# Kernel optimization log

Measured on AMD Instinct MI355X. Metric: run time of the kernel, lower is better.

The kernel has to match this reference:

```python
import jax, jax.numpy as jnp
import numpy as np

B, L, D = 2, 2048, 1024
H, DK, DV = 16, 64, 64
EPS = 1e-6


def setup_inputs() -> dict:
    key = jax.random.key(0)
    ks = jax.random.split(key, 7)
    s = 0.02
    return {
        "x": jax.random.normal(ks[0], (B, L, D), dtype=jnp.float32),
        "Wq": jax.random.normal(ks[1], (D, H * DK), dtype=jnp.float32) * s,
        "Wk": jax.random.normal(ks[2], (D, H * DK), dtype=jnp.float32) * s,
        "Wv": jax.random.normal(ks[3], (D, H * DV), dtype=jnp.float32) * s,
        "Wo": jax.random.normal(ks[4], (H * DV, D), dtype=jnp.float32) * s,
        "ln_gamma": jnp.ones((D,), dtype=jnp.float32),
        "ln_beta": jnp.zeros((D,), dtype=jnp.float32),
    }


def reference(x, Wq, Wk, Wv, Wo, ln_gamma, ln_beta):
    temp = jnp.asarray(DK, x.dtype) ** 0.5
    # projections -> [B, H, L, Dh]
    q = (x @ Wq).reshape(B, L, H, DK).transpose(0, 2, 1, 3)
    k = (x @ Wk).reshape(B, L, H, DK).transpose(0, 2, 1, 3)
    v = (x @ Wv).reshape(B, L, H, DV).transpose(0, 2, 1, 3)
    # naive attention: explicit [B,H,L,L] scores (dropout rate 0 -> identity)
    scores = jnp.einsum("bhqd,bhkd->bhqk", q / temp, k)
    attn = jax.nn.softmax(scores, axis=-1)
    o = jnp.einsum("bhqk,bhkd->bhqd", attn, v)
    o = o.transpose(0, 2, 1, 3).reshape(B, L, H * DV)
    out = o @ Wo + x  # residual
    # LayerNorm(eps=1e-6)
    mu = jnp.mean(out, axis=-1, keepdims=True)
    var = jnp.var(out, axis=-1, keepdims=True)
    return (out - mu) * jax.lax.rsqrt(var + EPS) * ln_gamma + ln_beta
```

## Files before the change

### kernel.cpp

```cpp
#include <hip/hip_runtime.h>


typedef __bf16 bf16;
typedef __bf16 bf16x2 __attribute__((ext_vector_type(2)));
typedef __bf16 bf16x4 __attribute__((ext_vector_type(4)));
typedef __bf16 bf16x8 __attribute__((ext_vector_type(8)));
typedef float floatx4 __attribute__((ext_vector_type(4)));
typedef int intx4 __attribute__((ext_vector_type(4)));

#define MFMA16(a, b, c) __builtin_amdgcn_mfma_f32_16x16x32_bf16((a), (b), (c), 0, 0, 0)

__device__ __forceinline__ void gll16(const bf16* g, bf16* l) {
  __builtin_amdgcn_global_load_lds((const __attribute__((address_space(1))) void*)g,
                                   (__attribute__((address_space(3))) void*)l, 16, 0, 0);
}

__global__ __launch_bounds__(256) void k_prep(const float* __restrict__ x,
                                              const float* __restrict__ Wq, const float* __restrict__ Wk,
                                              const float* __restrict__ Wv, const float* __restrict__ Wo,
                                              bf16* __restrict__ xb, bf16* __restrict__ WT) {
  __shared__ float tile[32][33];
  const int z = blockIdx.z;
  const int tx = threadIdx.x, ty = threadIdx.y;
  if (z < 4) {
    const float* W = (z == 0) ? Wq : (z == 1) ? Wk : (z == 2) ? Wv : Wo;
    const int n0 = blockIdx.x * 32, k0 = blockIdx.y * 32;
#pragma unroll
    for (int j = 0; j < 32; j += 8)
      tile[ty + j][tx] = W[(size_t)(k0 + ty + j) * 1024 + n0 + tx];
    __syncthreads();
#pragma unroll
    for (int j = 0; j < 32; j += 8)
      WT[(size_t)(z * 1024 + n0 + ty + j) * 1024 + k0 + tx] = (bf16)tile[tx][ty + j];
  } else {
    const int blin = blockIdx.y * 32 + blockIdx.x;
    const int tid = ty * 32 + tx;
    const size_t i = (((size_t)(z - 4) * 1024 + blin) * 256 + tid) * 4;
    const float4 v = *reinterpret_cast<const float4*>(x + i);
    bf16x4 o = {(bf16)v.x, (bf16)v.y, (bf16)v.z, (bf16)v.w};
    *reinterpret_cast<bf16x4*>(xb + i) = o;
  }
}

template <int MODE>
__global__ __launch_bounds__(256) void k_gemm(const bf16* __restrict__ A, const bf16* __restrict__ Bt,
                                              const float* __restrict__ X, float* __restrict__ Y,
                                              bf16* __restrict__ QB, bf16* __restrict__ KB,
                                              bf16* __restrict__ VTB) {
  __shared__ __align__(16) bf16 As[2 * 128 * 64];
  __shared__ __align__(16) bf16 Bs[2 * 128 * 64];
  const int t = threadIdx.x;
  const int lane = t & 63, wv = t >> 6;
  const int qd = lane >> 4, col = lane & 15;
  const int c7 = col & 7;
  const int wm = wv >> 1, wn = wv & 1;
  const int m0 = blockIdx.x * 128, n0 = blockIdx.y * 128;
  const int srow = wv * 8 + (lane >> 3);
  const int scol = ((lane & 7) ^ (lane >> 3)) * 8;
  const bf16* Ag = A + (size_t)(m0 + srow) * 1024 + scol;
  const bf16* Bg = Bt + (size_t)(n0 + srow) * 1024 + scol;

  floatx4 acc[4][4] = {};

#define GSTAGE(bu, ti)                                                                              \
  do {                                                                                              \
    _Pragma("unroll") for (int rd = 0; rd < 4; rd++) {                                              \
      gll16(Ag + (size_t)rd * 32 * 1024 + (ti) * 64, As + (bu) * 8192 + (rd * 32 + wv * 8) * 64);   \
      gll16(Bg + (size_t)rd * 32 * 1024 + (ti) * 64, Bs + (bu) * 8192 + (rd * 32 + wv * 8) * 64);   \
    }                                                                                               \
  } while (0)

#define GCOMP(bu)                                                                                   \
  do {                                                                                              \
    const bf16* as_ = As + (bu) * 8192;                                                             \
    const bf16* bs_ = Bs + (bu) * 8192;                                                             \
    _Pragma("unroll") for (int ks = 0; ks < 2; ks++) {                                              \
      bf16x8 af[4], bfr[4];                                                                         \
      _Pragma("unroll") for (int i = 0; i < 4; i++)                                                 \
        af[i] = *reinterpret_cast<const bf16x8*>(as_ + (wm * 64 + i * 16 + col) * 64 +              \
                                                 ((ks * 4 + qd) ^ c7) * 8);                         \
      _Pragma("unroll") for (int i = 0; i < 4; i++)                                                 \
        bfr[i] = *reinterpret_cast<const bf16x8*>(bs_ + (wn * 64 + i * 16 + col) * 64 +             \
                                                  ((ks * 4 + qd) ^ c7) * 8);                        \
      _Pragma("unroll") for (int i = 0; i < 4; i++)                                                 \
        _Pragma("unroll") for (int j = 0; j < 4; j++)                                               \
          acc[i][j] = MFMA16(af[i], bfr[j], acc[i][j]);                                             \
    }                                                                                               \
  } while (0)

  GSTAGE(0, 0);
  GSTAGE(1, 1);
  for (int ti = 0; ti < 14; ti += 2) {
    asm volatile("s_waitcnt vmcnt(8)" ::: "memory");
    __builtin_amdgcn_s_barrier();
    GCOMP(0);
    __builtin_amdgcn_s_barrier();
    if (ti + 2 < 16) GSTAGE(0, ti + 2);
    asm volatile("s_waitcnt vmcnt(8)" ::: "memory");
    __builtin_amdgcn_s_barrier();
    GCOMP(1);
    __builtin_amdgcn_s_barrier();
    if (ti + 3 < 16) GSTAGE(1, ti + 3);
  }
  asm volatile("s_waitcnt vmcnt(8)" ::: "memory");
  __builtin_amdgcn_s_barrier();
  GCOMP(0);
  asm volatile("s_waitcnt vmcnt(0)" ::: "memory");
  __builtin_amdgcn_s_barrier();
  GCOMP(1);
#undef GSTAGE
#undef GCOMP

#pragma unroll
  for (int i = 0; i < 4; i++) {
#pragma unroll
    for (int j = 0; j < 4; j++) {
      const int mb = m0 + wm * 64 + i * 16 + qd * 4;
      const int n = n0 + wn * 64 + j * 16 + col;
      if (MODE == 0) {
        const int seg = n >> 10;
        const int h = (n & 1023) >> 6, dd = n & 63;
#pragma unroll
        for (int r = 0; r < 4; r++) {
          const int m = mb + r;
          const int bb = m >> 11, l = m & 2047;
          const float v = acc[i][j][r];
          if (seg == 0)
            QB[((size_t)(bb * 16 + h) * 2048 + l) * 64 + dd] = (bf16)(v * 0.18033688f);
          else if (seg == 1)
            KB[((size_t)(bb * 16 + h) * 2048 + l) * 64 + dd] = (bf16)v;
          else
            VTB[((size_t)(bb * 16 + h) * 64 + dd) * 2048 + l] = (bf16)v;
        }
      } else {
#pragma unroll
        for (int r = 0; r < 4; r++) {
          const int m = mb + r;
          Y[(size_t)m * 1024 + n] = acc[i][j][r] + X[(size_t)m * 1024 + n];
        }
      }
    }
  }
}

__global__ __launch_bounds__(256) void k_gemm_op(const bf16* __restrict__ A, const bf16* __restrict__ Bt,
                                                 const float* __restrict__ X, float* __restrict__ Y) {
  __shared__ __align__(16) bf16 As[2 * 64 * 64];
  __shared__ __align__(16) bf16 Bs[2 * 128 * 64];
  const int t = threadIdx.x;
  const int lane = t & 63, wv = t >> 6;
  const int qd = lane >> 4, col = lane & 15;
  const int c7 = col & 7;
  const int wm = wv >> 1, wn = wv & 1;
  const int m0 = blockIdx.x * 64, n0 = blockIdx.y * 128;
  const int srow = wv * 8 + (lane >> 3);
  const int scol = ((lane & 7) ^ (lane >> 3)) * 8;
  const bf16* Ag = A + (size_t)(m0 + srow) * 1024 + scol;
  const bf16* Bg = Bt + (size_t)(n0 + srow) * 1024 + scol;

  floatx4 acc[2][4] = {};

#define GSTAGE(bu, ti)                                                                              \
  do {                                                                                              \
    _Pragma("unroll") for (int rd = 0; rd < 2; rd++)                                                \
      gll16(Ag + (size_t)rd * 32 * 1024 + (ti) * 64, As + (bu) * 4096 + (rd * 32 + wv * 8) * 64);   \
    _Pragma("unroll") for (int rd = 0; rd < 4; rd++)                                                \
      gll16(Bg + (size_t)rd * 32 * 1024 + (ti) * 64, Bs + (bu) * 8192 + (rd * 32 + wv * 8) * 64);   \
  } while (0)

#define GCOMP(bu)                                                                                   \
  do {                                                                                              \
    const bf16* as_ = As + (bu) * 4096;                                                             \
    const bf16* bs_ = Bs + (bu) * 8192;                                                             \
    _Pragma("unroll") for (int ks = 0; ks < 2; ks++) {                                              \
      bf16x8 af[2], bfr[4];                                                                         \
      _Pragma("unroll") for (int i = 0; i < 2; i++)                                                 \
        af[i] = *reinterpret_cast<const bf16x8*>(as_ + (wm * 32 + i * 16 + col) * 64 +              \
                                                 ((ks * 4 + qd) ^ c7) * 8);                         \
      _Pragma("unroll") for (int j = 0; j < 4; j++)                                                 \
        bfr[j] = *reinterpret_cast<const bf16x8*>(bs_ + (wn * 64 + j * 16 + col) * 64 +             \
                                                  ((ks * 4 + qd) ^ c7) * 8);                        \
      _Pragma("unroll") for (int i = 0; i < 2; i++)                                                 \
        _Pragma("unroll") for (int j = 0; j < 4; j++)                                               \
          acc[i][j] = MFMA16(af[i], bfr[j], acc[i][j]);                                             \
    }                                                                                               \
  } while (0)

  GSTAGE(0, 0);
  GSTAGE(1, 1);
  for (int ti = 0; ti < 14; ti += 2) {
    asm volatile("s_waitcnt vmcnt(6)" ::: "memory");
    __builtin_amdgcn_s_barrier();
    GCOMP(0);
    __builtin_amdgcn_s_barrier();
    if (ti + 2 < 16) GSTAGE(0, ti + 2);
    asm volatile("s_waitcnt vmcnt(6)" ::: "memory");
    __builtin_amdgcn_s_barrier();
    GCOMP(1);
    __builtin_amdgcn_s_barrier();
    if (ti + 3 < 16) GSTAGE(1, ti + 3);
  }
  asm volatile("s_waitcnt vmcnt(6)" ::: "memory");
  __builtin_amdgcn_s_barrier();
  GCOMP(0);
  asm volatile("s_waitcnt vmcnt(0)" ::: "memory");
  __builtin_amdgcn_s_barrier();
  GCOMP(1);
#undef GSTAGE
#undef GCOMP

#pragma unroll
  for (int i = 0; i < 2; i++) {
#pragma unroll
    for (int j = 0; j < 4; j++) {
      const int mb = m0 + wm * 32 + i * 16 + qd * 4;
      const int n = n0 + wn * 64 + j * 16 + col;
#pragma unroll
      for (int r = 0; r < 4; r++) {
        const int m = mb + r;
        Y[(size_t)m * 1024 + n] = acc[i][j][r] + X[(size_t)m * 1024 + n];
      }
    }
  }
}

__global__ __launch_bounds__(256) void k_attn(const bf16* __restrict__ QB, const bf16* __restrict__ KB,
                                              const bf16* __restrict__ VTB, bf16* __restrict__ OB) {
  __shared__ __align__(16) bf16 Ks[5][64 * 64];
  __shared__ __align__(16) bf16 Vs[5][64 * 64];
  const int t = threadIdx.x;
  const int lane = t & 63, wv = t >> 6;
  const int qd = lane >> 4, col = lane & 15;
  const int c7 = col & 7;
  const int bid = blockIdx.x;
  const int lin = (bid & 7) * 64 + (bid >> 3);
  const int bh = lin >> 4;
  const int qr = (lin & 15) * 128 + wv * 32;
  const int lrow0 = wv * 8 + (lane >> 3);
  const int scol = ((lane & 7) ^ (lane >> 3)) * 8;
  const int kg0 = ((lrow0 >> 5) << 5) + (((lrow0 >> 2) & 3) << 3) + (((lrow0 >> 4) & 1) << 2) + (lrow0 & 3);
  const int r1 = lrow0 + 32;
  const int kg1 = ((r1 >> 5) << 5) + (((r1 >> 2) & 3) << 3) + (((r1 >> 4) & 1) << 2) + (r1 & 3);
  const bf16* Kg0 = KB + ((size_t)bh * 2048 + kg0) * 64 + scol;
  const bf16* Kg1 = KB + ((size_t)bh * 2048 + kg1) * 64 + scol;
  const bf16* Vg0 = VTB + ((size_t)bh * 64 + lrow0) * 2048 + scol;
  const bf16* Vg1 = VTB + ((size_t)bh * 64 + lrow0 + 32) * 2048 + scol;

  bf16x8 bQ[2][2];
#pragma unroll
  for (int qt = 0; qt < 2; qt++)
#pragma unroll
    for (int s = 0; s < 2; s++)
      bQ[qt][s] = *reinterpret_cast<const bf16x8*>(QB + ((size_t)bh * 2048 + qr + qt * 16 + col) * 64 + s * 32 + qd * 8);

  bf16x8 bOnes;
#pragma unroll
  for (int i = 0; i < 8; i++) bOnes[i] = (bf16)1.0f;

  floatx4 oacc[2][4] = {};
  floatx4 lacc[2] = {};
  floatx4 scur[2][4];
  int pk[2][4][2];

#define STAGE(bu, ti)                                                  \
  do {                                                                 \
    gll16(Kg0 + (size_t)(ti) * 4096, &Ks[bu][(wv * 8) * 64]);          \
    gll16(Kg1 + (size_t)(ti) * 4096, &Ks[bu][(32 + wv * 8) * 64]);     \
    gll16(Vg0 + (ti) * 64, &Vs[bu][(wv * 8) * 64]);                    \
    gll16(Vg1 + (ti) * 64, &Vs[bu][(32 + wv * 8) * 64]);               \
  } while (0)

#define QK(bu)                                                                                      \
  do {                                                                                              \
    const bf16* ks_ = Ks[bu];                                                                       \
    _Pragma("unroll") for (int nt = 0; nt < 4; nt++) {                                              \
      bf16x8 a0 = *reinterpret_cast<const bf16x8*>(ks_ + (nt * 16 + col) * 64 + (qd ^ c7) * 8);     \
      bf16x8 a1 = *reinterpret_cast<const bf16x8*>(ks_ + (nt * 16 + col) * 64 + ((4 + qd) ^ c7) * 8); \
      _Pragma("unroll") for (int qt = 0; qt < 2; qt++) {                                            \
        floatx4 zz = {0.f, 0.f, 0.f, 0.f};                                                          \
        zz = MFMA16(a0, bQ[qt][0], zz);                                                             \
        zz = MFMA16(a1, bQ[qt][1], zz);                                                             \
        scur[qt][nt] = zz;                                                                          \
      }                                                                                             \
    }                                                                                               \
  } while (0)

#define EXPPACK()                                                                               \
  do {                                                                                          \
    _Pragma("unroll") for (int qt = 0; qt < 2; qt++) {                                          \
      _Pragma("unroll") for (int nt = 0; nt < 4; nt++) {                                        \
        const float e0 = __builtin_amdgcn_exp2f(scur[qt][nt][0]);                               \
        const float e1 = __builtin_amdgcn_exp2f(scur[qt][nt][1]);                               \
        const float e2 = __builtin_amdgcn_exp2f(scur[qt][nt][2]);                               \
        const float e3 = __builtin_amdgcn_exp2f(scur[qt][nt][3]);                               \
        bf16x2 p01, p23;                                                                        \
        p01[0] = (bf16)e0; p01[1] = (bf16)e1;                                                   \
        p23[0] = (bf16)e2; p23[1] = (bf16)e3;                                                   \
        pk[qt][nt][0] = __builtin_bit_cast(int, p01);                                           \
        pk[qt][nt][1] = __builtin_bit_cast(int, p23);                                           \
      }                                                                                         \
    }                                                                                           \
  } while (0)

#define PV(bu)                                                                                      \
  do {                                                                                              \
    const bf16* vs_ = Vs[bu];                                                                       \
    bf16x8 bV[4][2];                                                                                \
    _Pragma("unroll") for (int nd = 0; nd < 4; nd++) {                                              \
      bV[nd][0] = *reinterpret_cast<const bf16x8*>(vs_ + (nd * 16 + col) * 64 + (qd ^ c7) * 8);     \
      bV[nd][1] = *reinterpret_cast<const bf16x8*>(vs_ + (nd * 16 + col) * 64 + ((4 + qd) ^ c7) * 8); \
    }                                                                                               \
    _Pragma("unroll") for (int qt = 0; qt < 2; qt++) {                                              \
      _Pragma("unroll") for (int s = 0; s < 2; s++) {                                               \
        intx4 w;                                                                                    \
        w[0] = pk[qt][2 * s][0]; w[1] = pk[qt][2 * s][1];                                           \
        w[2] = pk[qt][2 * s + 1][0]; w[3] = pk[qt][2 * s + 1][1];                                   \
        const bf16x8 aP = __builtin_bit_cast(bf16x8, w);                                            \
        _Pragma("unroll") for (int nd = 0; nd < 4; nd++)                                            \
          oacc[qt][nd] = MFMA16(aP, bV[nd][s], oacc[qt][nd]);                                       \
        lacc[qt] = MFMA16(aP, bOnes, lacc[qt]);                  \
      }                                                                                             \
    }                                                                                               \
  } while (0)

#define ITER5(cur, prv, stg, ti)                                       \
  do {                                                                 \
    asm volatile("s_waitcnt vmcnt(8)" ::: "memory");                   \
    __builtin_amdgcn_s_barrier();                                      \
    STAGE(stg, ((ti) + 3 <= 31) ? ((ti) + 3) : 31);                    \
    EXPPACK();                                                         \
    __builtin_amdgcn_s_setprio(1);                                     \
    QK(cur);                                                           \
    PV(prv);                                                           \
    __builtin_amdgcn_s_setprio(0);                                     \
  } while (0)

  STAGE(0, 0);
  STAGE(1, 1);
  STAGE(2, 2);
  STAGE(3, 3);
  asm volatile("s_waitcnt vmcnt(12)" ::: "memory");
  __builtin_amdgcn_s_barrier();
  QK(0);
  for (int j = 1; j < 30; j += 5) {
    ITER5(1, 0, 4, j);
    ITER5(2, 1, 0, j + 1);
    ITER5(3, 2, 1, j + 2);
    ITER5(4, 3, 2, j + 3);
    ITER5(0, 4, 3, j + 4);
  }
  ITER5(1, 0, 4, 31);
  EXPPACK();
  __builtin_amdgcn_s_setprio(1);
  PV(1);
  __builtin_amdgcn_s_setprio(0);

  const int bb = bh >> 4, h = bh & 15;
#pragma unroll
  for (int qt = 0; qt < 2; qt++) {
#pragma unroll
    for (int r = 0; r < 4; r++) {
      const float linv = 1.f / lacc[qt][r];
      const size_t m = (size_t)bb * 2048 + qr + qt * 16 + qd * 4 + r;
#pragma unroll
      for (int nd = 0; nd < 4; nd++)
        OB[m * 1024 + h * 64 + nd * 16 + col] = (bf16)(oacc[qt][nd][r] * linv);
    }
  }
#undef STAGE
#undef QK
#undef EXPPACK
#undef PV
#undef ITER5
}

__global__ __launch_bounds__(256) void k_ln(const float* __restrict__ Yin, const float* __restrict__ gamma,
                                            const float* __restrict__ beta, float* __restrict__ out) {
  __shared__ float red[8];
  const int row = blockIdx.x, t = threadIdx.x;
  const float4 v = *reinterpret_cast<const float4*>(Yin + (size_t)row * 1024 + t * 4);
  float s = v.x + v.y + v.z + v.w;
  float ss = v.x * v.x + v.y * v.y + v.z * v.z + v.w * v.w;
#pragma unroll
  for (int d = 1; d < 64; d <<= 1) {
    s += __shfl_xor(s, d);
    ss += __shfl_xor(ss, d);
  }
  if ((t & 63) == 0) {
    red[t >> 6] = s;
    red[4 + (t >> 6)] = ss;
  }
  __syncthreads();
  s = red[0] + red[1] + red[2] + red[3];
  ss = red[4] + red[5] + red[6] + red[7];
  const float mu = s * (1.f / 1024.f);
  const float var = ss * (1.f / 1024.f) - mu * mu;
  const float rs = rsqrtf(var + 1e-6f);
  const float4 g = *reinterpret_cast<const float4*>(gamma + t * 4);
  const float4 bt = *reinterpret_cast<const float4*>(beta + t * 4);
  float4 o;
  o.x = (v.x - mu) * rs * g.x + bt.x;
  o.y = (v.y - mu) * rs * g.y + bt.y;
  o.z = (v.z - mu) * rs * g.z + bt.z;
  o.w = (v.w - mu) * rs * g.w + bt.w;
  *reinterpret_cast<float4*>(out + (size_t)row * 1024 + t * 4) = o;
}

extern "C" void kernel_launch(void* const* d_in, const int* in_sizes, int n_in,
                              void* d_out, int out_size, void* d_ws, size_t ws_size,
                              hipStream_t stream) {
  (void)in_sizes; (void)n_in; (void)out_size; (void)ws_size;
  const float* x = (const float*)d_in[0];
  const float* Wq = (const float*)d_in[1];
  const float* Wk = (const float*)d_in[2];
  const float* Wv = (const float*)d_in[3];
  const float* Wo = (const float*)d_in[4];
  const float* gamma = (const float*)d_in[5];
  const float* beta = (const float*)d_in[6];

  char* ws = (char*)d_ws;
  const size_t MB = 1ull << 20;
  bf16* XB = (bf16*)(ws);
  bf16* OB = (bf16*)(ws);
  bf16* WT = (bf16*)(ws + 8 * MB);
  bf16* QB = (bf16*)(ws + 16 * MB);
  bf16* KB = (bf16*)(ws + 24 * MB);
  bf16* VTB = (bf16*)(ws + 32 * MB);
  float* Y = (float*)(ws + 16 * MB);

  k_prep<<<dim3(32, 32, 8), dim3(32, 8), 0, stream>>>(x, Wq, Wk, Wv, Wo, XB, WT);
  k_gemm<0><<<dim3(32, 24), 256, 0, stream>>>(XB, WT, nullptr, nullptr, QB, KB, VTB);
  k_attn<<<512, 256, 0, stream>>>(QB, KB, VTB, OB);
  k_gemm_op<<<dim3(64, 8), 256, 0, stream>>>(OB, WT + (size_t)3072 * 1024, x, Y);
  k_ln<<<4096, 256, 0, stream>>>(Y, gamma, beta, (float*)d_out);
}
```

Before: 186.2 us.

## Enlarge QKV GEMM tile to 256x256 with 512 threads and 4-stage pipeline

Rewrites the QKV projection GEMM to use 256x256 block tiles with 8 waves, each wave owning a 128x64 output sub-tile. K is split into 32-wide slices across a 4-buffer LDS ring with a new swizzle, and each iteration uses a single barrier with prefetch issued before compute. This raises arithmetic intensity per block and cuts barrier count, at the cost of a 192-block grid that underfills the 256 CUs and higher register pressure from 32 accumulators.

```diff
diff --git a/kernel.cpp b/kernel.cpp
--- a/kernel.cpp
+++ b/kernel.cpp
@@ -42,31 +42,30 @@
   }
 }
 
-template <int MODE>
-__global__ __launch_bounds__(256) void k_gemm(const bf16* __restrict__ A, const bf16* __restrict__ Bt,
-                                              const float* __restrict__ X, float* __restrict__ Y,
-                                              bf16* __restrict__ QB, bf16* __restrict__ KB,
-                                              bf16* __restrict__ VTB) {
-  __shared__ __align__(16) bf16 As[2 * 128 * 64];
-  __shared__ __align__(16) bf16 Bs[2 * 128 * 64];
+__global__ __launch_bounds__(512) void k_gemm_qkv(const bf16* __restrict__ A, const bf16* __restrict__ Bt,
+                                                  bf16* __restrict__ QB, bf16* __restrict__ KB,
+                                                  bf16* __restrict__ VTB) {
+  __shared__ __align__(16) bf16 As[4 * 8192];
+  __shared__ __align__(16) bf16 Bs[4 * 8192];
   const int t = threadIdx.x;
   const int lane = t & 63, wv = t >> 6;
   const int qd = lane >> 4, col = lane & 15;
-  const int c7 = col & 7;
-  const int wm = wv >> 1, wn = wv & 1;
-  const int m0 = blockIdx.x * 128, n0 = blockIdx.y * 128;
-  const int srow = wv * 8 + (lane >> 3);
-  const int scol = ((lane & 7) ^ (lane >> 3)) * 8;
+  const int wm = wv >> 2, wn = wv & 3;
+  const int m0 = blockIdx.x * 256, n0 = blockIdx.y * 256;
+  const int u = (lane & 7) ^ (lane >> 3);
+  const int srow = wv * 16 + ((lane >> 3) << 1) + (u >> 2);
+  const int scol = (u & 3) * 8;
   const bf16* Ag = A + (size_t)(m0 + srow) * 1024 + scol;
   const bf16* Bg = Bt + (size_t)(n0 + srow) * 1024 + scol;
-
-  floatx4 acc[4][4] = {};
+  const int sl = (qd + ((col & 1) << 2)) ^ ((col >> 1) & 7);
+
+  floatx4 acc[8][4] = {};
 
 #define GSTAGE(bu, ti)                                                                              \
   do {                                                                                              \
-    _Pragma("unroll") for (int rd = 0; rd < 4; rd++) {                                              \
-      gll16(Ag + (size_t)rd * 32 * 1024 + (ti) * 64, As + (bu) * 8192 + (rd * 32 + wv * 8) * 64);   \
-      gll16(Bg + (size_t)rd * 32 * 1024 + (ti) * 64, Bs + (bu) * 8192 + (rd * 32 + wv * 8) * 64);   \
+    _Pragma("unroll") for (int rd = 0; rd < 2; rd++) {                                              \
+      gll16(Ag + (size_t)rd * 128 * 1024 + (ti) * 32, As + (bu) * 8192 + rd * 4096 + wv * 512);     \
+      gll16(Bg + (size_t)rd * 128 * 1024 + (ti) * 32, Bs + (bu) * 8192 + rd * 4096 + wv * 512);     \
     }                                                                                               \
   } while (0)
 
@@ -74,70 +73,63 @@
   do {                                                                                              \
     const bf16* as_ = As + (bu) * 8192;                                                             \
     const bf16* bs_ = Bs + (bu) * 8192;                                                             \
-    _Pragma("unroll") for (int ks = 0; ks < 2; ks++) {                                              \
-      bf16x8 af[4], bfr[4];                                                                         \
-      _Pragma("unroll") for (int i = 0; i < 4; i++)                                                 \
-        af[i] = *reinterpret_cast<const bf16x8*>(as_ + (wm * 64 + i * 16 + col) * 64 +              \
-                                                 ((ks * 4 + qd) ^ c7) * 8);                         \
-      _Pragma("unroll") for (int i = 0; i < 4; i++)                                                 \
-        bfr[i] = *reinterpret_cast<const bf16x8*>(bs_ + (wn * 64 + i * 16 + col) * 64 +             \
-                                                  ((ks * 4 + qd) ^ c7) * 8);                        \
-      _Pragma("unroll") for (int i = 0; i < 4; i++)                                                 \
-        _Pragma("unroll") for (int j = 0; j < 4; j++)                                               \
-          acc[i][j] = MFMA16(af[i], bfr[j], acc[i][j]);                                             \
-    }                                                                                               \
+    bf16x8 af[8], bfr[4];                                                                           \
+    _Pragma("unroll") for (int i = 0; i < 8; i++)                                                   \
+      af[i] = *reinterpret_cast<const bf16x8*>(as_ + (wm * 64 + i * 8 + (col >> 1)) * 64 + sl * 8); \
+    _Pragma("unroll") for (int j = 0; j < 4; j++)                                                   \
+      bfr[j] = *reinterpret_cast<const bf16x8*>(bs_ + (wn * 32 + j * 8 + (col >> 1)) * 64 + sl * 8);\
+    _Pragma("unroll") for (int i = 0; i < 8; i++)                                                   \
+      _Pragma("unroll") for (int j = 0; j < 4; j++)                                                 \
+        acc[i][j] = MFMA16(af[i], bfr[j], acc[i][j]);                                               \
+  } while (0)
+
+#define GITER(cb, sb, ti)                                              \
+  do {                                                                 \
+    asm volatile("s_waitcnt vmcnt(4)" ::: "memory");                   \
+    __builtin_amdgcn_s_barrier();                                      \
+    GSTAGE(sb, (ti) + 2);                                              \
+    GCOMP(cb);                                                         \
   } while (0)
 
   GSTAGE(0, 0);
   GSTAGE(1, 1);
-  for (int ti = 0; ti < 14; ti += 2) {
-    asm volatile("s_waitcnt vmcnt(8)" ::: "memory");
-    __builtin_amdgcn_s_barrier();
-    GCOMP(0);
-    __builtin_amdgcn_s_barrier();
-    if (ti + 2 < 16) GSTAGE(0, ti + 2);
-    asm volatile("s_waitcnt vmcnt(8)" ::: "memory");
-    __builtin_amdgcn_s_barrier();
-    GCOMP(1);
-    __builtin_amdgcn_s_barrier();
-    if (ti + 3 < 16) GSTAGE(1, ti + 3);
-  }
-  asm volatile("s_waitcnt vmcnt(8)" ::: "memory");
+  for (int ti = 0; ti < 28; ti += 4) {
+    GITER(0, 2, ti);
+    GITER(1, 3, ti + 1);
+    GITER(2, 0, ti + 2);
+    GITER(3, 1, ti + 3);
+  }
+  GITER(0, 2, 28);
+  GITER(1, 3, 29);
+  asm volatile("s_waitcnt vmcnt(4)" ::: "memory");
   __builtin_amdgcn_s_barrier();
-  GCOMP(0);
+  GCOMP(2);
   asm volatile("s_waitcnt vmcnt(0)" ::: "memory");
   __builtin_amdgcn_s_barrier();
-  GCOMP(1);
+  GCOMP(3);
 #undef GSTAGE
 #undef GCOMP
-
-#pragma unroll
-  for (int i = 0; i < 4; i++) {
+#undef GITER
+
+#pragma unroll
+  for (int i = 0; i < 8; i++) {
 #pragma unroll
     for (int j = 0; j < 4; j++) {
-      const int mb = m0 + wm * 64 + i * 16 + qd * 4;
+      const int mb = m0 + wm * 128 + i * 16 + qd * 4;
       const int n = n0 + wn * 64 + j * 16 + col;
-      if (MODE == 0) {
-        const int seg = n >> 10;
-        const int h = (n & 1023) >> 6, dd = n & 63;
-#pragma unroll
-        for (int r = 0; r < 4; r++) {
-          const int m = mb + r;
-          const int bb = m >> 11, l = m & 2047;
-          const float v = acc[i][j][r];
-          if (seg == 0)
-            QB[((size_t)(bb * 16 + h) * 2048 + l) * 64 + dd] = (bf16)(v * 0.18033688f);
-          else if (seg == 1)
-            KB[((size_t)(bb * 16 + h) * 2048 + l) * 64 + dd] = (bf16)v;
-          else
-            VTB[((size_t)(bb * 16 + h) * 64 + dd) * 2048 + l] = (bf16)v;
-        }
-      } else {
-#pragma unroll
-        for (int r = 0; r < 4; r++) {
-          const int m = mb + r;
-          Y[(size_t)m * 1024 + n] = acc[i][j][r] + X[(size_t)m * 1024 + n];
-        }
+      const int seg = n >> 10;
+      const int h = (n & 1023) >> 6, dd = n & 63;
+#pragma unroll
+      for (int r = 0; r < 4; r++) {
+        const int m = mb + r;
+        const int bb = m >> 11, l = m & 2047;
+        const float v = acc[i][j][r];
+        if (seg == 0)
+          QB[((size_t)(bb * 16 + h) * 2048 + l) * 64 + dd] = (bf16)(v * 0.18033688f);
+        else if (seg == 1)
+          KB[((size_t)(bb * 16 + h) * 2048 + l) * 64 + dd] = (bf16)v;
+        else
+          VTB[((size_t)(bb * 16 + h) * 64 + dd) * 2048 + l] = (bf16)v;
       }
     }
   }
@@ -429,7 +421,7 @@
   float* Y = (float*)(ws + 16 * MB);
 
   k_prep<<<dim3(32, 32, 8), dim3(32, 8), 0, stream>>>(x, Wq, Wk, Wv, Wo, XB, WT);
-  k_gemm<0><<<dim3(32, 24), 256, 0, stream>>>(XB, WT, nullptr, nullptr, QB, KB, VTB);
+  k_gemm_qkv<<<dim3(16, 12), 512, 0, stream>>>(XB, WT, QB, KB, VTB);
   k_attn<<<512, 256, 0, stream>>>(QB, KB, VTB, OB);
   k_gemm_op<<<dim3(64, 8), 256, 0, stream>>>(OB, WT + (size_t)3072 * 1024, x, Y);
   k_ln<<<4096, 256, 0, stream>>>(Y, gamma, beta, (float*)d_out);
```

Result: slower. 198.4 us (+6.5%).
